# Kernel tuning notes

Measured on AMD Instinct MI355X. Metric: run time of the kernel, lower is better.

## Reference

```python
import jax, jax.numpy as jnp
from jax import lax
import numpy as np

N = 262144      # rays (512x512 image)
H = 64          # SDF MLP hidden width
LAT = 32        # latent size
NEAR = 0.2
FAR = 2.0
EPS = 1e-3
ITERS = 192     # eval-mode sphere_march iterations


def mlp_sdf(p, W0, b0, W1, b1, W2, b2):
    # p: [..., 3] -> [..., 1+LAT]; col 0 = signed distance, cols 1: = latent
    h = jax.nn.relu(p @ W0 + b0)
    h = jax.nn.relu(h @ W1 + b1)
    return h @ W2 + b2


def sphere_march(sdf, r_o, r_d):
    n = r_o.shape[0]
    hits = jnp.zeros((n,), bool)
    rem = jnp.ones((n,), bool)
    cd = jnp.full((n,), NEAR, jnp.float32)

    def body(i, state):
        hits, rem, cd = state
        d = sdf(r_o + r_d * cd[:, None])[:, 0]
        # hits[rem] |= (dist < eps) & (curr_dist[rem] <= far)
        hits = hits | (rem & (d < EPS) & (cd <= FAR))
        # curr_dist[rem] += dist
        cd = jnp.where(rem, cd + d, cd)
        # rem[hits | (curr_dist > far)] = False
        rem = rem & ~(hits | (cd > FAR))
        return hits, rem, cd

    hits, rem, cd = lax.fori_loop(0, ITERS, body, (hits, rem, cd))
    pts = r_o + r_d * cd[:, None]
    return pts, hits, cd


def setup_inputs() -> dict:
    key = jax.random.key(0)
    ks = jax.random.split(key, 12)
    r_o = 0.1 * jax.random.normal(ks[0], (N, 3), jnp.float32)
    r_d = jax.random.normal(ks[1], (N, 3), jnp.float32)
    r_d = r_d / jnp.linalg.norm(r_d, axis=-1, keepdims=True)
    lin = lambda k, i, o: jax.random.normal(k, (i, o), jnp.float32) / np.sqrt(i)
    FEAT = 3 + 3 + 3 + LAT  # x, view, normal, latent
    return {
        "rays": jnp.concatenate([r_o, r_d], axis=-1),
        "W0": lin(ks[2], 3, H), "b0": jnp.zeros((H,), jnp.float32),
        "W1": lin(ks[3], H, H), "b1": jnp.zeros((H,), jnp.float32),
        "W2": lin(ks[4], H, 1 + LAT), "b2": jnp.zeros((1 + LAT,), jnp.float32),
        "RW0": lin(ks[5], FEAT, H), "Rb0": jnp.zeros((H,), jnp.float32),
        "RW1": lin(ks[6], H, 3), "Rb1": jnp.zeros((3,), jnp.float32),
    }


def reference(rays, W0, b0, W1, b1, W2, b2, RW0, Rb0, RW1, Rb1):
    r_o, r_d = rays[:, :3], rays[:, 3:]
    sdf = lambda p: mlp_sdf(p, W0, b0, W1, b1, W2, b2)

    pts, hit, t = sphere_march(sdf, r_o, r_d)          # [N,3], [N], [N]

    latent = sdf(pts)[:, 1:]                            # [N, LAT]

    # normals = d sdf_value / d pts (SDFModel.normals via autograd)
    val, vjp_fn = jax.vjp(lambda p: mlp_sdf(p, W0, b0, W1, b1, W2, b2)[:, 0], pts)
    (nrm,) = vjp_fn(jnp.ones_like(val))                 # [N,3]
    nrm = jnp.where(hit[:, None], nrm, 0.0)

    # reflectance(x=pts, view=r_d, normal=n, latent=latent)
    feat = jnp.concatenate([pts, r_d, nrm, latent], axis=-1)
    rgb = jax.nn.sigmoid(jax.nn.relu(feat @ RW0 + Rb0) @ RW1 + Rb1)

    # out[hit] = refl(...); zeros elsewhere
    return jnp.where(hit[:, None], rgb, 0.0)
```

## Files before the change

kernel.cpp:

```cpp
#include <hip/hip_runtime.h>
#include <math.h>

#define NRAYS 262144
#define MAXIT 192
#define NEARV 0.2f
#define FARV  2.0f
#define EPSV  0.001f
#define KCHUNK 16
#define NROUNDS 12

__device__ __forceinline__ float sdf_eval(
    float px, float py, float pz,
    const float* __restrict__ W0, const float* __restrict__ b0,
    const float* __restrict__ W1, const float* __restrict__ b1,
    const float* __restrict__ W2, float b2_0)
{
    float h1[64];
    #pragma unroll
    for (int j = 0; j < 64; ++j) h1[j] = 0.f;

    for (int k = 0; k < 64; ++k) {
        float z = px * W0[k] + py * W0[64 + k] + pz * W0[128 + k];
        z += b0[k];
        const float a = fmaxf(z, 0.f);
        #pragma unroll
        for (int j = 0; j < 64; ++j) h1[j] = fmaf(a, W1[k * 64 + j], h1[j]);
    }

    float d = 0.f;
    #pragma unroll
    for (int j = 0; j < 64; ++j)
        d = fmaf(fmaxf(h1[j] + b1[j], 0.f), W2[j * 33], d);
    return d + b2_0;
}

__global__ __launch_bounds__(256, 2)
void march_round(const float* __restrict__ rays,
                 const float* __restrict__ W0, const float* __restrict__ b0,
                 const float* __restrict__ W1, const float* __restrict__ b1,
                 const float* __restrict__ W2, const float* __restrict__ b2,
                 int round0, int it_base,
                 const int* __restrict__ in_cnt,
                 const int* __restrict__ in_idx, const float* __restrict__ in_cd,
                 int* __restrict__ out_cnt,
                 int* __restrict__ out_idx, float* __restrict__ out_cd,
                 float* __restrict__ t_out,
                 int* __restrict__ hitq, int* __restrict__ hit_cnt)
{
    const int i    = blockIdx.x * 256 + threadIdx.x;
    const int lane = threadIdx.x & 63;
    const int n    = round0 ? NRAYS : *in_cnt;

    bool alive = (i < n);
    bool hit   = false;
    int  ridx  = 0;
    float cd   = NEARV;
    int  it    = it_base;

    if (alive) {
        if (round0) {
            ridx = i;
        } else {
            ridx = in_idx[i];
            cd   = in_cd[i];
        }
    }
    if (__ballot(alive) == 0ull) return;

    const float* r = rays + (size_t)ridx * 6;
    const float ox = r[0], oy = r[1], oz = r[2];
    const float rdx = r[3], rdy = r[4], rdz = r[5];
    const float b2_0 = b2[0];

    for (int s = 0; s < KCHUNK; ++s) {
        if (__ballot(alive) == 0ull) break;

        const float px = ox + rdx * cd;
        const float py = oy + rdy * cd;
        const float pz = oz + rdz * cd;

        const float d = sdf_eval(px, py, pz, W0, b0, W1, b1, W2, b2_0);

        if (alive) {
            ++it;
            if (d < EPSV && cd <= FARV) hit = true;
            cd += d;
            if (hit || cd > FARV || it >= MAXIT) {
                t_out[ridx] = cd;
                if (hit) {
                    const int p = atomicAdd(hit_cnt, 1);
                    hitq[p] = ridx;
                }
                alive = false;
            }
        }
    }

    const unsigned long long m = __ballot(alive);
    if (m != 0ull) {
        const int leader = __builtin_ctzll(m);
        int base = 0;
        if (lane == leader) base = atomicAdd(out_cnt, __builtin_popcountll(m));
        base = __shfl(base, leader);
        if (alive) {
            const int off = __builtin_popcountll(m & ((1ull << lane) - 1ull));
            out_idx[base + off] = ridx;
            out_cd[base + off]  = cd;
        }
    }
}

__global__ __launch_bounds__(256, 2)
void shade_hit(const float* __restrict__ rays,
               const float* __restrict__ W0, const float* __restrict__ b0,
               const float* __restrict__ W1, const float* __restrict__ b1,
               const float* __restrict__ W2, const float* __restrict__ b2,
               const float* __restrict__ RW0, const float* __restrict__ Rb0,
               const float* __restrict__ RW1, const float* __restrict__ Rb1,
               const float* __restrict__ t_in,
               const int* __restrict__ hitq, const int* __restrict__ hit_cnt,
               float* __restrict__ out)
{
    const int n = *hit_cnt;
    if (blockIdx.x * 256 >= n) return;

    __shared__ float sW0[3 * 64];
    __shared__ float sb0[64];
    __shared__ float sW1[64 * 64];
    __shared__ float sb1[64];
    __shared__ float sW2T[33 * 64];
    __shared__ float sb2[33];
    __shared__ float sRW0T[64 * 48];
    __shared__ float sRb0[64];
    __shared__ float sRW1[64 * 3];
    __shared__ float sRb1[3];

    const int tid = threadIdx.x;
    for (int i = tid; i < 3 * 64; i += 256) sW0[i] = W0[i];
    for (int i = tid; i < 64 * 64; i += 256) sW1[i] = W1[i];
    for (int i = tid; i < 33 * 64; i += 256) {
        const int c = i >> 6, j = i & 63;
        sW2T[i] = W2[j * 33 + c];
    }
    for (int i = tid; i < 64 * 41; i += 256) {
        const int u = i / 41, f = i - u * 41;
        sRW0T[u * 48 + f] = RW0[f * 64 + u];
    }
    if (tid < 64) { sb0[tid] = b0[tid]; sb1[tid] = b1[tid]; sRb0[tid] = Rb0[tid]; }
    if (tid < 33) sb2[tid] = b2[tid];
    if (tid < 192) sRW1[tid] = RW1[tid];
    if (tid < 3) sRb1[tid] = Rb1[tid];
    __syncthreads();

    const int qi = blockIdx.x * 256 + tid;
    if (qi >= n) return;
    const int i = hitq[qi];

    const float* r = rays + (size_t)i * 6;
    const float cd = t_in[i];
    const float ox = r[0], oy = r[1], oz = r[2];
    const float dx = r[3], dy = r[4], dz = r[5];
    const float px = ox + dx * cd;
    const float py = oy + dy * cd;
    const float pz = oz + dz * cd;

    float h1[64];
    #pragma unroll
    for (int j = 0; j < 64; ++j) h1[j] = 0.f;

    for (int k = 0; k < 64; ++k) {
        float z = px * sW0[k] + py * sW0[64 + k] + pz * sW0[128 + k];
        z += sb0[k];
        const float a = fmaxf(z, 0.f);
        #pragma unroll
        for (int j = 0; j < 64; ++j) h1[j] = fmaf(a, sW1[k * 64 + j], h1[j]);
    }
    #pragma unroll
    for (int j = 0; j < 64; ++j) h1[j] = fmaxf(h1[j] + sb1[j], 0.f);

    float lat[32];
    #pragma unroll
    for (int c = 1; c < 33; ++c) {
        float acc = 0.f;
        #pragma unroll
        for (int j = 0; j < 64; ++j) acc = fmaf(h1[j], sW2T[c * 64 + j], acc);
        lat[c - 1] = acc + sb2[c];
    }

    #pragma unroll
    for (int j = 0; j < 64; ++j) h1[j] = (h1[j] > 0.f) ? sW2T[j] : 0.f;

    float nx = 0.f, ny = 0.f, nz = 0.f;
    for (int k = 0; k < 64; ++k) {
        float z = px * sW0[k] + py * sW0[64 + k] + pz * sW0[128 + k];
        z += sb0[k];
        float g = 0.f;
        #pragma unroll
        for (int j = 0; j < 64; ++j) g = fmaf(h1[j], sW1[k * 64 + j], g);
        if (z > 0.f) {
            nx = fmaf(g, sW0[k], nx);
            ny = fmaf(g, sW0[64 + k], ny);
            nz = fmaf(g, sW0[128 + k], nz);
        }
    }

    float r0 = 0.f, r1 = 0.f, r2 = 0.f;
    for (int u = 0; u < 64; ++u) {
        const float* w = &sRW0T[u * 48];
        float a = px * w[0] + py * w[1] + pz * w[2];
        a = fmaf(dx, w[3], a); a = fmaf(dy, w[4], a); a = fmaf(dz, w[5], a);
        a = fmaf(nx, w[6], a); a = fmaf(ny, w[7], a); a = fmaf(nz, w[8], a);
        #pragma unroll
        for (int q = 0; q < 32; ++q) a = fmaf(lat[q], w[9 + q], a);
        a += sRb0[u];
        const float ru = fmaxf(a, 0.f);
        r0 = fmaf(ru, sRW1[u * 3 + 0], r0);
        r1 = fmaf(ru, sRW1[u * 3 + 1], r1);
        r2 = fmaf(ru, sRW1[u * 3 + 2], r2);
    }
    r0 += sRb1[0]; r1 += sRb1[1]; r2 += sRb1[2];

    out[i * 3 + 0] = 1.f / (1.f + expf(-r0));
    out[i * 3 + 1] = 1.f / (1.f + expf(-r1));
    out[i * 3 + 2] = 1.f / (1.f + expf(-r2));
}

__global__ __launch_bounds__(256, 2)
void march_kernel(const float* __restrict__ rays,
                  const float* __restrict__ W0, const float* __restrict__ b0,
                  const float* __restrict__ W1, const float* __restrict__ b1,
                  const float* __restrict__ W2, const float* __restrict__ b2,
                  float* __restrict__ t_out, int* __restrict__ hit_out,
                  int* __restrict__ counter)
{
    float ox = 0.f, oy = 0.f, oz = 0.f, rdx = 0.f, rdy = 0.f, rdz = 0.f;
    float cd = 0.f;
    int ridx = -1, it = 0;
    bool has = false, hit = false, exhausted = false;

    const float b2_0 = b2[0];

    while (true) {
        if (!has && !exhausted) {
            int idx = atomicAdd(counter, 1);
            if (idx < NRAYS) {
                const float* r = rays + (size_t)idx * 6;
                ox = r[0]; oy = r[1]; oz = r[2];
                rdx = r[3]; rdy = r[4]; rdz = r[5];
                cd = NEARV; it = 0; hit = false; has = true; ridx = idx;
            } else {
                exhausted = true;
            }
        }
        if (__ballot(has) == 0ull) break;

        const float px = ox + rdx * cd;
        const float py = oy + rdy * cd;
        const float pz = oz + rdz * cd;

        const float d = sdf_eval(px, py, pz, W0, b0, W1, b1, W2, b2_0);

        if (has) {
            ++it;
            if (d < EPSV && cd <= FARV) hit = true;
            cd += d;
            if (hit || cd > FARV || it >= MAXIT) {
                t_out[ridx] = cd;
                hit_out[ridx] = hit ? 1 : 0;
                has = false;
            }
        }
    }
}

__global__ __launch_bounds__(256, 2)
void shade_kernel(const float* __restrict__ rays,
                  const float* __restrict__ W0, const float* __restrict__ b0,
                  const float* __restrict__ W1, const float* __restrict__ b1,
                  const float* __restrict__ W2, const float* __restrict__ b2,
                  const float* __restrict__ RW0, const float* __restrict__ Rb0,
                  const float* __restrict__ RW1, const float* __restrict__ Rb1,
                  const float* __restrict__ t_in, const int* __restrict__ hit_in,
                  float* __restrict__ out)
{
    __shared__ float sW0[3 * 64];
    __shared__ float sb0[64];
    __shared__ float sW1[64 * 64];
    __shared__ float sb1[64];
    __shared__ float sW2T[33 * 64];
    __shared__ float sb2[33];
    __shared__ float sRW0T[64 * 48];
    __shared__ float sRb0[64];
    __shared__ float sRW1[64 * 3];
    __shared__ float sRb1[3];

    const int tid = threadIdx.x;
    for (int i = tid; i < 3 * 64; i += 256) sW0[i] = W0[i];
    for (int i = tid; i < 64 * 64; i += 256) sW1[i] = W1[i];
    for (int i = tid; i < 33 * 64; i += 256) {
        const int c = i >> 6, j = i & 63;
        sW2T[i] = W2[j * 33 + c];
    }
    for (int i = tid; i < 64 * 41; i += 256) {
        const int u = i / 41, f = i - u * 41;
        sRW0T[u * 48 + f] = RW0[f * 64 + u];
    }
    if (tid < 64) { sb0[tid] = b0[tid]; sb1[tid] = b1[tid]; sRb0[tid] = Rb0[tid]; }
    if (tid < 33) sb2[tid] = b2[tid];
    if (tid < 192) sRW1[tid] = RW1[tid];
    if (tid < 3) sRb1[tid] = Rb1[tid];
    __syncthreads();

    const int i = blockIdx.x * 256 + tid;
    const bool hit = hit_in[i] != 0;

    if (__ballot(hit) == 0ull) {
        out[i * 3 + 0] = 0.f;
        out[i * 3 + 1] = 0.f;
        out[i * 3 + 2] = 0.f;
        return;
    }

    const float* r = rays + (size_t)i * 6;
    const float cd = t_in[i];
    const float ox = r[0], oy = r[1], oz = r[2];
    const float dx = r[3], dy = r[4], dz = r[5];
    const float px = ox + dx * cd;
    const float py = oy + dy * cd;
    const float pz = oz + dz * cd;

    float h1[64];
    #pragma unroll
    for (int j = 0; j < 64; ++j) h1[j] = 0.f;

    for (int k = 0; k < 64; ++k) {
        float z = px * sW0[k] + py * sW0[64 + k] + pz * sW0[128 + k];
        z += sb0[k];
        const float a = fmaxf(z, 0.f);
        #pragma unroll
        for (int j = 0; j < 64; ++j) h1[j] = fmaf(a, sW1[k * 64 + j], h1[j]);
    }
    #pragma unroll
    for (int j = 0; j < 64; ++j) h1[j] = fmaxf(h1[j] + sb1[j], 0.f);

    float lat[32];
    #pragma unroll
    for (int c = 1; c < 33; ++c) {
        float acc = 0.f;
        #pragma unroll
        for (int j = 0; j < 64; ++j) acc = fmaf(h1[j], sW2T[c * 64 + j], acc);
        lat[c - 1] = acc + sb2[c];
    }

    #pragma unroll
    for (int j = 0; j < 64; ++j) h1[j] = (h1[j] > 0.f) ? sW2T[j] : 0.f;

    float nx = 0.f, ny = 0.f, nz = 0.f;
    for (int k = 0; k < 64; ++k) {
        float z = px * sW0[k] + py * sW0[64 + k] + pz * sW0[128 + k];
        z += sb0[k];
        float g = 0.f;
        #pragma unroll
        for (int j = 0; j < 64; ++j) g = fmaf(h1[j], sW1[k * 64 + j], g);
        if (z > 0.f) {
            nx = fmaf(g, sW0[k], nx);
            ny = fmaf(g, sW0[64 + k], ny);
            nz = fmaf(g, sW0[128 + k], nz);
        }
    }
    if (!hit) { nx = 0.f; ny = 0.f; nz = 0.f; }

    float r0 = 0.f, r1 = 0.f, r2 = 0.f;
    for (int u = 0; u < 64; ++u) {
        const float* w = &sRW0T[u * 48];
        float a = px * w[0] + py * w[1] + pz * w[2];
        a = fmaf(dx, w[3], a); a = fmaf(dy, w[4], a); a = fmaf(dz, w[5], a);
        a = fmaf(nx, w[6], a); a = fmaf(ny, w[7], a); a = fmaf(nz, w[8], a);
        #pragma unroll
        for (int q = 0; q < 32; ++q) a = fmaf(lat[q], w[9 + q], a);
        a += sRb0[u];
        const float ru = fmaxf(a, 0.f);
        r0 = fmaf(ru, sRW1[u * 3 + 0], r0);
        r1 = fmaf(ru, sRW1[u * 3 + 1], r1);
        r2 = fmaf(ru, sRW1[u * 3 + 2], r2);
    }
    r0 += sRb1[0]; r1 += sRb1[1]; r2 += sRb1[2];

    const float o0 = 1.f / (1.f + expf(-r0));
    const float o1 = 1.f / (1.f + expf(-r1));
    const float o2 = 1.f / (1.f + expf(-r2));

    out[i * 3 + 0] = hit ? o0 : 0.f;
    out[i * 3 + 1] = hit ? o1 : 0.f;
    out[i * 3 + 2] = hit ? o2 : 0.f;
}

extern "C" void kernel_launch(void* const* d_in, const int* in_sizes, int n_in,
                              void* d_out, int out_size, void* d_ws, size_t ws_size,
                              hipStream_t stream) {
    const float* rays = (const float*)d_in[0];
    const float* W0   = (const float*)d_in[1];
    const float* b0   = (const float*)d_in[2];
    const float* W1   = (const float*)d_in[3];
    const float* b1   = (const float*)d_in[4];
    const float* W2   = (const float*)d_in[5];
    const float* b2   = (const float*)d_in[6];
    const float* RW0  = (const float*)d_in[7];
    const float* Rb0  = (const float*)d_in[8];
    const float* RW1  = (const float*)d_in[9];
    const float* Rb1  = (const float*)d_in[10];

    const size_t need = (size_t)(16 + 6 * NRAYS) * 4;

    if (ws_size >= need) {
        int*   cnt  = (int*)d_ws;
        float* t_ws = (float*)d_ws + 16;
        int*   qiA  = (int*)d_ws + 16 + (size_t)NRAYS;
        float* qcA  = (float*)d_ws + 16 + 2 * (size_t)NRAYS;
        int*   qiB  = (int*)d_ws + 16 + 3 * (size_t)NRAYS;
        float* qcB  = (float*)d_ws + 16 + 4 * (size_t)NRAYS;
        int*   hitq = (int*)d_ws + 16 + 5 * (size_t)NRAYS;

        hipMemsetAsync(cnt, 0, 16 * sizeof(int), stream);
        hipMemsetAsync(d_out, 0, (size_t)out_size, stream);

        march_round<<<NRAYS / 256, 256, 0, stream>>>(
            rays, W0, b0, W1, b1, W2, b2,
            1, 0, nullptr, nullptr, nullptr,
            &cnt[0], qiA, qcA, t_ws, hitq, &cnt[15]);

        for (int r2 = 1; r2 < NROUNDS; ++r2) {
            const int*   icnt = &cnt[r2 - 1];
            int*         ocnt = &cnt[r2];
            const int*   ii = (r2 & 1) ? qiA : qiB;
            const float* ic = (r2 & 1) ? qcA : qcB;
            int*         oi = (r2 & 1) ? qiB : qiA;
            float*       oc = (r2 & 1) ? qcB : qcA;
            march_round<<<NRAYS / 256, 256, 0, stream>>>(
                rays, W0, b0, W1, b1, W2, b2,
                0, r2 * KCHUNK, icnt, ii, ic,
                ocnt, oi, oc, t_ws, hitq, &cnt[15]);
        }

        shade_hit<<<NRAYS / 256, 256, 0, stream>>>(
            rays, W0, b0, W1, b1, W2, b2, RW0, Rb0, RW1, Rb1,
            t_ws, hitq, &cnt[15], (float*)d_out);
    } else {
        float* t_ws  = (float*)d_ws;
        int*   hit_ws = (int*)d_ws + NRAYS;
        int*   ctr    = (int*)d_ws + 2 * NRAYS;

        hipMemsetAsync(ctr, 0, sizeof(int), stream);
        march_kernel<<<1024, 256, 0, stream>>>(rays, W0, b0, W1, b1, W2, b2,
                                               t_ws, hit_ws, ctr);
        shade_kernel<<<NRAYS / 256, 256, 0, stream>>>(rays, W0, b0, W1, b1, W2, b2,
                                                      RW0, Rb0, RW1, Rb1,
                                                      t_ws, hit_ws, (float*)d_out);
    }
}
```

Measured before the change: 3.972 ms.

## Lockstep march waves with block barriers and larger blocks for weight reuse

```diff
diff --git a/kernel.cpp b/kernel.cpp
--- a/kernel.cpp
+++ b/kernel.cpp
@@ -8,6 +8,7 @@
 #define EPSV  0.001f
 #define KCHUNK 16
 #define NROUNDS 12
+#define MBLK 512
 
 __device__ __forceinline__ float sdf_eval(
     float px, float py, float pz,
@@ -34,7 +35,7 @@
     return d + b2_0;
 }
 
-__global__ __launch_bounds__(256, 2)
+__global__ __launch_bounds__(MBLK, 4)
 void march_round(const float* __restrict__ rays,
                  const float* __restrict__ W0, const float* __restrict__ b0,
                  const float* __restrict__ W1, const float* __restrict__ b1,
@@ -47,9 +48,11 @@
                  float* __restrict__ t_out,
                  int* __restrict__ hitq, int* __restrict__ hit_cnt)
 {
-    const int i    = blockIdx.x * 256 + threadIdx.x;
+    const int i    = blockIdx.x * MBLK + threadIdx.x;
     const int lane = threadIdx.x & 63;
     const int n    = round0 ? NRAYS : *in_cnt;
+
+    if (blockIdx.x * MBLK >= n) return;
 
     bool alive = (i < n);
     bool hit   = false;
@@ -65,7 +68,6 @@
             cd   = in_cd[i];
         }
     }
-    if (__ballot(alive) == 0ull) return;
 
     const float* r = rays + (size_t)ridx * 6;
     const float ox = r[0], oy = r[1], oz = r[2];
@@ -73,13 +75,33 @@
     const float b2_0 = b2[0];
 
     for (int s = 0; s < KCHUNK; ++s) {
-        if (__ballot(alive) == 0ull) break;
-
         const float px = ox + rdx * cd;
         const float py = oy + rdy * cd;
         const float pz = oz + rdz * cd;
 
-        const float d = sdf_eval(px, py, pz, W0, b0, W1, b1, W2, b2_0);
+        float h1[64];
+        #pragma unroll
+        for (int j = 0; j < 64; ++j) h1[j] = 0.f;
+
+        for (int kt = 0; kt < 8; ++kt) {
+            #pragma unroll
+            for (int kk = 0; kk < 8; ++kk) {
+                const int k = kt * 8 + kk;
+                float z = px * W0[k] + py * W0[64 + k] + pz * W0[128 + k];
+                z += b0[k];
+                const float a = fmaxf(z, 0.f);
+                #pragma unroll
+                for (int j = 0; j < 64; ++j)
+                    h1[j] = fmaf(a, W1[k * 64 + j], h1[j]);
+            }
+            __builtin_amdgcn_s_barrier();
+        }
+
+        float d = 0.f;
+        #pragma unroll
+        for (int j = 0; j < 64; ++j)
+            d = fmaf(fmaxf(h1[j] + b1[j], 0.f), W2[j * 33], d);
+        d += b2_0;
 
         if (alive) {
             ++it;
@@ -424,7 +446,9 @@
         hipMemsetAsync(cnt, 0, 16 * sizeof(int), stream);
         hipMemsetAsync(d_out, 0, (size_t)out_size, stream);
 
-        march_round<<<NRAYS / 256, 256, 0, stream>>>(
+        const int blocks = NRAYS / MBLK;
+
+        march_round<<<blocks, MBLK, 0, stream>>>(
             rays, W0, b0, W1, b1, W2, b2,
             1, 0, nullptr, nullptr, nullptr,
             &cnt[0], qiA, qcA, t_ws, hitq, &cnt[15]);
@@ -436,7 +460,7 @@
             const float* ic = (r2 & 1) ? qcA : qcB;
             int*         oi = (r2 & 1) ? qiB : qiA;
             float*       oc = (r2 & 1) ? qcB : qcA;
-            march_round<<<NRAYS / 256, 256, 0, stream>>>(
+            march_round<<<blocks, MBLK, 0, stream>>>(
                 rays, W0, b0, W1, b1, W2, b2,
                 0, r2 * KCHUNK, icnt, ii, ic,
                 ocnt, oi, oc, t_ws, hitq, &cnt[15]);
```

Measured after the change: 4.484 ms. 1.13x slower.
